# Optimization experiments

Hardware: AMD Instinct MI355X
Metric: run time of the kernel (lower is better)

Reference implementation:

```python
import jax, jax.numpy as jnp
import numpy as np

NEG_SLOPE = 0.01  # PyTorch LeakyReLU default


def leaky(x):
    return jnp.where(x >= 0, x, NEG_SLOPE * x)


def conv(x, w, b, stride, pad):
    # x: NCHW, w: OIHW
    y = jax.lax.conv_general_dilated(
        x, w, (stride, stride), [(pad, pad), (pad, pad)],
        dimension_numbers=("NCHW", "OIHW", "NCHW"))
    return y + b[None, :, None, None]


def conv_transpose(x, w, b, stride, pad):
    # w has PyTorch ConvTranspose2d layout (in, out, kh, kw)
    wf = jnp.flip(w, (2, 3)).transpose(1, 0, 2, 3)  # -> (out, in, kh, kw)
    k = w.shape[2]
    p = k - 1 - pad
    y = jax.lax.conv_general_dilated(
        x, wf, (1, 1), [(p, p), (p, p)], lhs_dilation=(stride, stride),
        dimension_numbers=("NCHW", "OIHW", "NCHW"))
    return y + b[None, :, None, None]


def setup_inputs() -> dict:
    key = jax.random.key(0)
    ks = jax.random.split(key, 16)
    D, K = 64, 512
    s = 0.05
    inp = {
        "x": jax.random.normal(ks[0], (64, 1, 128, 128), jnp.float32),
        # encoder
        "ew1": jax.random.normal(ks[1], (8, 1, 4, 4), jnp.float32) * s,
        "eb1": jnp.zeros((8,), jnp.float32),
        "ew2": jax.random.normal(ks[2], (16, 8, 4, 4), jnp.float32) * s,
        "eb2": jnp.zeros((16,), jnp.float32),
        "ew3": jax.random.normal(ks[3], (16, 16, 3, 3), jnp.float32) * s,
        "eb3": jnp.zeros((16,), jnp.float32),
        "ew4": jax.random.normal(ks[4], (D, 16, 1, 1), jnp.float32) * s,
        "eb4": jnp.zeros((D,), jnp.float32),
        # codebook, init uniform(-1/K, 1/K) as in the module
        "codebook": jax.random.uniform(ks[5], (K, D), jnp.float32, -1.0 / K, 1.0 / K),
        # decoder
        "dw1": jax.random.normal(ks[6], (16, D, 3, 3), jnp.float32) * s,
        "db1": jnp.zeros((16,), jnp.float32),
        "dw2": jax.random.normal(ks[7], (16, 8, 4, 4), jnp.float32) * s,  # ConvT (in,out,k,k)
        "db2": jnp.zeros((8,), jnp.float32),
        "dw3": jax.random.normal(ks[8], (8, 1, 4, 4), jnp.float32) * s,  # ConvT (in,out,k,k)
        "db3": jnp.zeros((1,), jnp.float32),
    }
    return inp


BETA = 0.25


def vq(latents_nchw, codebook):
    # latents -> NHWC
    lat = jnp.transpose(latents_nchw, (0, 2, 3, 1))
    shp = lat.shape
    D = shp[-1]
    flat = lat.reshape(-1, D)  # [M, D]
    # pairwise squared distances to codebook [M, K]
    dist = (jnp.sum(flat ** 2, axis=1, keepdims=True)
            + jnp.sum(codebook ** 2, axis=1)
            - 2.0 * flat @ codebook.T)
    inds = jnp.argmin(dist, axis=1)  # [M]
    quant = codebook[inds].reshape(shp)  # gather == one-hot @ codebook
    commitment_loss = jnp.mean((jax.lax.stop_gradient(quant) - lat) ** 2)
    embedding_loss = jnp.mean((quant - jax.lax.stop_gradient(lat)) ** 2)
    vq_loss = commitment_loss * BETA + embedding_loss
    # straight-through estimator
    quant = lat + jax.lax.stop_gradient(quant - lat)
    return jnp.transpose(quant, (0, 3, 1, 2)), vq_loss


def reference(x, ew1, eb1, ew2, eb2, ew3, eb3, ew4, eb4, codebook,
              dw1, db1, dw2, db2, dw3, db3):
    # encoder
    h = leaky(conv(x, ew1, eb1, 2, 1))
    h = leaky(conv(h, ew2, eb2, 2, 1))
    h = leaky(conv(h, ew3, eb3, 1, 1))
    h = leaky(conv(h, ew4, eb4, 1, 0))
    # vector quantization
    q, vq_loss = vq(h, codebook)
    # decoder
    d = leaky(conv(q, dw1, db1, 1, 1))
    d = leaky(conv_transpose(d, dw2, db2, 2, 1))
    d = jnp.tanh(conv_transpose(d, dw3, db3, 2, 1))
    return d, vq_loss
```

## Files before the change

### kernel.cpp

```cpp
#include <hip/hip_runtime.h>
#include <math.h>

#define DEV __device__ __forceinline__
DEV float leakyf(float v) { return v >= 0.f ? v : 0.01f * v; }
DEV int rfl(int v) { return __builtin_amdgcn_readfirstlane(v); }

struct F4 { float x, y, z, w; };

#define OFF_XP   0u
#define OFF_H1P  1081600u
#define OFF_H2P  3311872u
#define OFF_H3   4495616u
#define OFF_D1P  5544192u
#define OFF_D2P  6727936u
#define OFF_IDX  8958208u
#define OFF_U    9023744u
#define OFF_C2   9097472u
#define OFF_W4T  9097984u
#define OFF_DWT  9099008u
#define OFF_LOSS 9108224u

__global__ void prep_k(const float* __restrict__ ew4, const float* __restrict__ dw1,
                       const float* __restrict__ cb, float* __restrict__ ws)
{
    int b = blockIdx.x, t = threadIdx.x;
    if (b < 4) {
        int id = b * 256 + t;
        int d = id & 63, ci = id >> 6;
        ws[OFF_W4T + id] = ew4[d * 16 + ci];
    } else if (b < 6) {
        int k = (b - 4) * 256 + t;
        float s = 0.f;
        #pragma unroll
        for (int d = 0; d < 64; ++d) { float v = cb[k * 64 + d]; s = fmaf(v, v, s); }
        ws[OFF_C2 + k] = s;
    } else {
        int id = (b - 6) * 256 + t;
        if (id < 9216) {
            int co = id & 15, tap = (id >> 4) % 9, ci = id / 144;
            ws[OFF_DWT + id] = dw1[(co * 64 + ci) * 9 + tap];
        }
    }
}

__global__ void uprep_k(const float* __restrict__ dwT, const float* __restrict__ cb,
                        float* __restrict__ U)
{
    int id = blockIdx.x * 256 + threadIdx.x;
    int k = id / 144;
    int r = id - k * 144;
    float s = 0.f;
    #pragma unroll
    for (int ci = 0; ci < 64; ++ci)
        s = fmaf(cb[k * 64 + ci], dwT[ci * 144 + r], s);
    U[id] = s;
}

DEV void halo_store(float* base, int plane, int r, int W, int H, long psz)
{
    int row, col;
    if (r < W)          { row = 0;     col = r; }
    else if (r < 2 * W) { row = H - 1; col = r - W; }
    else { int r2 = r - 2 * W; row = 1 + (r2 >> 1); col = (r2 & 1) ? W - 1 : 0; }
    base[plane * psz + row * W + col] = 0.f;
}

__global__ void halo_k(float* __restrict__ ws)
{
    int id = blockIdx.x * 256 + threadIdx.x;
    if (id < 33024) {
        halo_store(ws + OFF_XP, id / 516, id % 516, 130, 130, 16900);
    } else if (id < 166144) {
        int i = id - 33024;
        halo_store(ws + OFF_H1P, i / 260, i % 260, 66, 66, 4356);
    } else if (id < 301312) {
        int i = id - 166144;
        halo_store(ws + OFF_H2P, i / 132, i % 132, 34, 34, 1156);
    } else if (id < 436480) {
        int i = id - 301312;
        halo_store(ws + OFF_D1P, i / 132, i % 132, 34, 34, 1156);
    } else if (id < 569600) {
        int i = id - 436480;
        halo_store(ws + OFF_D2P, i / 260, i % 260, 66, 66, 4356);
    }
}

__global__ void padx_k(const float* __restrict__ x, float* __restrict__ xp)
{
    int id = blockIdx.x * 256 + threadIdx.x;
    int ix = id & 127, iy = (id >> 7) & 127, n = id >> 14;
    xp[(n * 130 + iy + 1) * 130 + ix + 1] = x[id];
}

__global__ __launch_bounds__(256) void e1p_k(const float* __restrict__ xp,
                                             const float* __restrict__ ew1,
                                             const float* __restrict__ eb1,
                                             float* __restrict__ h1p)
{
    __shared__ float wl[128];
    int t = threadIdx.x;
    if (t < 128) { int co = t & 7, tap = t >> 3; wl[t] = ew1[co * 16 + tap]; }
    __syncthreads();
    int id = blockIdx.x * 256 + t;
    int x = id & 63, y = (id >> 6) & 63, n = id >> 12;
    float acc[8];
    #pragma unroll
    for (int j = 0; j < 8; ++j) acc[j] = eb1[j];
    const float* base = xp + (n * 130 + 2 * y) * 130 + 2 * x;
    #pragma unroll
    for (int ky = 0; ky < 4; ++ky) {
        F4 v = *(const F4*)(base + ky * 130);
        float vv[4] = { v.x, v.y, v.z, v.w };
        #pragma unroll
        for (int kx = 0; kx < 4; ++kx) {
            const float* wp = &wl[(ky * 4 + kx) * 8];
            #pragma unroll
            for (int j = 0; j < 8; ++j) acc[j] = fmaf(vv[kx], wp[j], acc[j]);
        }
    }
    #pragma unroll
    for (int j = 0; j < 8; ++j)
        h1p[((n * 8 + j) * 66 + y + 1) * 66 + x + 1] = leakyf(acc[j]);
}

__global__ __launch_bounds__(256) void e2p_k(const float* __restrict__ h1p,
                                             const float* __restrict__ ew2,
                                             const float* __restrict__ eb2,
                                             float* __restrict__ h2p)
{
    __shared__ float wl[512];
    int t = threadIdx.x;
    int id = blockIdx.x * 256 + t;
    int x = id & 31, y = (id >> 5) & 31;
    int cg = rfl((id >> 10) & 3), n = id >> 12;
    {
        int i = t + (t < 256 ? 0 : 0);
        for (i = t; i < 512; i += 256) {
            int co = i & 3, r = i >> 2;
            int kx = r & 3, ky = (r >> 2) & 3, ci = r >> 4;
            wl[i] = ew2[((cg * 4 + co) * 8 + ci) * 16 + ky * 4 + kx];
        }
    }
    __syncthreads();
    float acc[4];
    #pragma unroll
    for (int j = 0; j < 4; ++j) acc[j] = eb2[cg * 4 + j];
    #pragma unroll 1
    for (int ci = 0; ci < 8; ++ci) {
        const float* base = h1p + ((n * 8 + ci) * 66 + 2 * y) * 66 + 2 * x;
        #pragma unroll
        for (int ky = 0; ky < 4; ++ky) {
            F4 v = *(const F4*)(base + ky * 66);
            float vv[4] = { v.x, v.y, v.z, v.w };
            #pragma unroll
            for (int kx = 0; kx < 4; ++kx) {
                const float* wp = &wl[((ci * 4 + ky) * 4 + kx) * 4];
                acc[0] = fmaf(vv[kx], wp[0], acc[0]);
                acc[1] = fmaf(vv[kx], wp[1], acc[1]);
                acc[2] = fmaf(vv[kx], wp[2], acc[2]);
                acc[3] = fmaf(vv[kx], wp[3], acc[3]);
            }
        }
    }
    #pragma unroll
    for (int j = 0; j < 4; ++j)
        h2p[((n * 16 + cg * 4 + j) * 34 + y + 1) * 34 + x + 1] = leakyf(acc[j]);
}

__global__ __launch_bounds__(256) void e3p_k(const float* __restrict__ h2p,
                                             const float* __restrict__ ew3,
                                             const float* __restrict__ eb3,
                                             float* __restrict__ h3)
{
    __shared__ float wl[576];
    int t = threadIdx.x;
    int id = blockIdx.x * 256 + t;
    int x = id & 31, y = (id >> 5) & 31;
    int cg = rfl((id >> 10) & 3), n = id >> 12;
    for (int i = t; i < 576; i += 256) {
        int co = i & 3, r = i >> 2;
        int kx = r % 3, ky = (r / 3) % 3, ci = r / 9;
        wl[i] = ew3[((cg * 4 + co) * 16 + ci) * 9 + ky * 3 + kx];
    }
    __syncthreads();
    float acc[4];
    #pragma unroll
    for (int j = 0; j < 4; ++j) acc[j] = eb3[cg * 4 + j];
    #pragma unroll 1
    for (int ci = 0; ci < 16; ++ci) {
        const float* base = h2p + ((n * 16 + ci) * 34 + y) * 34 + x;
        #pragma unroll
        for (int ky = 0; ky < 3; ++ky) {
            F4 v = *(const F4*)(base + ky * 34);
            float vv[3] = { v.x, v.y, v.z };
            #pragma unroll
            for (int kx = 0; kx < 3; ++kx) {
                const float* wp = &wl[((ci * 3 + ky) * 3 + kx) * 4];
                acc[0] = fmaf(vv[kx], wp[0], acc[0]);
                acc[1] = fmaf(vv[kx], wp[1], acc[1]);
                acc[2] = fmaf(vv[kx], wp[2], acc[2]);
                acc[3] = fmaf(vv[kx], wp[3], acc[3]);
            }
        }
    }
    #pragma unroll
    for (int j = 0; j < 4; ++j)
        h3[((n * 16 + cg * 4 + j) << 10) + (y << 5) + x] = leakyf(acc[j]);
}

__global__ __launch_bounds__(256) void vqh_k(const float* __restrict__ h3,
                                             const float* __restrict__ w4t,
                                             const float* __restrict__ eb4,
                                             const float* __restrict__ cb,
                                             const float* __restrict__ c2,
                                             int* __restrict__ idxOut,
                                             float* __restrict__ lossAcc)
{
    __shared__ float Fs[64 * 128];
    __shared__ float Cs[64 * 128];
    int t = threadIdx.x;
    int row0 = blockIdx.x << 7;
    int n = row0 >> 10;
    int pos0 = row0 & 1023;

    {
        int row = t & 127, dh = t >> 7;
        const float* hp = h3 + (n << 14) + pos0 + row;
        float h[16];
        #pragma unroll
        for (int ci = 0; ci < 16; ++ci) h[ci] = hp[ci << 10];
        #pragma unroll
        for (int q = 0; q < 8; ++q) {
            int d0 = dh * 32 + q * 4;
            float a0 = eb4[d0 + 0], a1 = eb4[d0 + 1];
            float a2 = eb4[d0 + 2], a3 = eb4[d0 + 3];
            #pragma unroll
            for (int ci = 0; ci < 16; ++ci) {
                float v = h[ci];
                const float* wp = w4t + (ci << 6) + d0;
                a0 = fmaf(v, wp[0], a0); a1 = fmaf(v, wp[1], a1);
                a2 = fmaf(v, wp[2], a2); a3 = fmaf(v, wp[3], a3);
            }
            Fs[(d0 + 0) * 128 + row] = leakyf(a0);
            Fs[(d0 + 1) * 128 + row] = leakyf(a1);
            Fs[(d0 + 2) * 128 + row] = leakyf(a2);
            Fs[(d0 + 3) * 128 + row] = leakyf(a3);
        }
    }

    int tr = t & 15, tc = t >> 4;
    float best[8]; int bk[8];
    #pragma unroll
    for (int i = 0; i < 8; ++i) { best[i] = 3.4e38f; bk[i] = 0; }

    #pragma unroll 1
    for (int p = 0; p < 4; ++p) {
        __syncthreads();
        {
            int code = t >> 1, dh = t & 1;
            const float* src = cb + (((p << 7) + code) << 6) + dh * 32;
            #pragma unroll
            for (int q = 0; q < 8; ++q) {
                float4 v = *(const float4*)(src + q * 4);
                int d0 = dh * 32 + q * 4;
                Cs[(d0 + 0) * 128 + code] = v.x;
                Cs[(d0 + 1) * 128 + code] = v.y;
                Cs[(d0 + 2) * 128 + code] = v.z;
                Cs[(d0 + 3) * 128 + code] = v.w;
            }
        }
        __syncthreads();

        float acc[8][8];
        #pragma unroll
        for (int i = 0; i < 8; ++i)
            #pragma unroll
            for (int j = 0; j < 8; ++j) acc[i][j] = 0.f;

        const float* fp0 = &Fs[tr * 4];
        const float* fp1 = &Fs[64 + tr * 4];
        const float* cp0 = &Cs[tc * 4];
        const float* cp1 = &Cs[64 + tc * 4];
        #pragma unroll 8
        for (int d = 0; d < 64; ++d) {
            float4 f0 = *(const float4*)(fp0 + d * 128);
            float4 f1 = *(const float4*)(fp1 + d * 128);
            float4 c0 = *(const float4*)(cp0 + d * 128);
            float4 c1 = *(const float4*)(cp1 + d * 128);
            float f[8] = { f0.x, f0.y, f0.z, f0.w, f1.x, f1.y, f1.z, f1.w };
            float c[8] = { c0.x, c0.y, c0.z, c0.w, c1.x, c1.y, c1.z, c1.w };
            #pragma unroll
            for (int i = 0; i < 8; ++i)
                #pragma unroll
                for (int j = 0; j < 8; ++j)
                    acc[i][j] = fmaf(f[i], c[j], acc[i][j]);
        }
        #pragma unroll
        for (int j = 0; j < 8; ++j) {
            int kk = (p << 7) + (j < 4 ? tc * 4 + j : 64 + tc * 4 + j - 4);
            float hc2 = 0.5f * c2[kk];
            #pragma unroll
            for (int i = 0; i < 8; ++i) {
                float s = hc2 - acc[i][j];
                if (s < best[i]) { best[i] = s; bk[i] = kk; }
            }
        }
    }

    __syncthreads();
    float* redS = Cs;
    int*   redI = (int*)(Cs + 2176);
    #pragma unroll
    for (int i = 0; i < 8; ++i) {
        int row = (i < 4) ? tr * 4 + i : 64 + tr * 4 + i - 4;
        redS[row * 17 + tc] = best[i];
        redI[row * 17 + tc] = bk[i];
    }
    __syncthreads();
    if (t < 128) {
        int row = t;
        float bs = redS[row * 17]; int bi = redI[row * 17];
        #pragma unroll
        for (int c = 1; c < 16; ++c) {
            float s2 = redS[row * 17 + c];
            int   i2 = redI[row * 17 + c];
            if (s2 < bs || (s2 == bs && i2 < bi)) { bs = s2; bi = i2; }
        }
        idxOut[row0 + row] = bi;
        const float* cr = cb + (bi << 6);
        float rs = 0.f;
        #pragma unroll
        for (int d = 0; d < 64; ++d) {
            float e = cr[d] - Fs[d * 128 + row];
            rs = fmaf(e, e, rs);
        }
        #pragma unroll
        for (int off = 32; off; off >>= 1) rs += __shfl_down(rs, off, 64);
        if ((t & 63) == 0) atomicAdd(lossAcc, rs);
    }
}

__global__ __launch_bounds__(256) void d1p_k(const int* __restrict__ idx,
                                             const float* __restrict__ U,
                                             const float* __restrict__ db1,
                                             float* __restrict__ d1p)
{
    int id = blockIdx.x * 256 + threadIdx.x;
    int x = id & 31, y = (id >> 5) & 31;
    int cg = rfl((id >> 10) & 3), n = id >> 12;
    float acc[4];
    #pragma unroll
    for (int j = 0; j < 4; ++j) acc[j] = db1[cg * 4 + j];
    const float4* U4 = (const float4*)U;
    #pragma unroll
    for (int tap = 0; tap < 9; ++tap) {
        int yy = y + tap / 3 - 1, xx = x + tap % 3 - 1;
        if (yy < 0 || yy > 31 || xx < 0 || xx > 31) continue;
        int k = idx[(n << 10) + (yy << 5) + xx];
        float4 u = U4[(k * 9 + tap) * 4 + cg];
        acc[0] += u.x; acc[1] += u.y; acc[2] += u.z; acc[3] += u.w;
    }
    #pragma unroll
    for (int j = 0; j < 4; ++j)
        d1p[((n * 16 + cg * 4 + j) * 34 + y + 1) * 34 + x + 1] = leakyf(acc[j]);
}

__global__ __launch_bounds__(256) void dt2p_k(const float* __restrict__ d1p,
                                              const float* __restrict__ dw2,
                                              const float* __restrict__ db2,
                                              float* __restrict__ d2p)
{
    __shared__ float wl[512];
    int t = threadIdx.x;
    int id = blockIdx.x * 256 + t;
    int x = id & 31, y = (id >> 5) & 31;
    int cg = rfl((id >> 10) & 3), n = id >> 12;
    for (int i = t; i < 512; i += 256) {
        int co = i & 1, tap = (i >> 1) & 15, ci = i >> 5;
        wl[i] = dw2[(ci * 8 + cg * 2 + co) * 16 + tap];
    }
    __syncthreads();
    float acc[2][2][2];
    #pragma unroll
    for (int py = 0; py < 2; ++py)
        #pragma unroll
        for (int px = 0; px < 2; ++px)
            #pragma unroll
            for (int j = 0; j < 2; ++j) acc[py][px][j] = db2[cg * 2 + j];
    #pragma unroll 1
    for (int ci = 0; ci < 16; ++ci) {
        const float* base = d1p + ((n * 16 + ci) * 34 + y) * 34 + x;
        F4 r0 = *(const F4*)(base);
        F4 r1 = *(const F4*)(base + 34);
        F4 r2 = *(const F4*)(base + 68);
        float v[3][3] = { { r0.x, r0.y, r0.z },
                          { r1.x, r1.y, r1.z },
                          { r2.x, r2.y, r2.z } };
        #pragma unroll
        for (int ky = 0; ky < 4; ++ky) {
            int py = (ky + 1) & 1;
            int dy = (ky == 0) ? 1 : (ky == 3 ? -1 : 0);
            #pragma unroll
            for (int kx = 0; kx < 4; ++kx) {
                int px = (kx + 1) & 1;
                int dx = (kx == 0) ? 1 : (kx == 3 ? -1 : 0);
                float vv = v[dy + 1][dx + 1];
                const float* wp = &wl[(ci * 16 + ky * 4 + kx) * 2];
                acc[py][px][0] = fmaf(vv, wp[0], acc[py][px][0]);
                acc[py][px][1] = fmaf(vv, wp[1], acc[py][px][1]);
            }
        }
    }
    #pragma unroll
    for (int py = 0; py < 2; ++py)
        #pragma unroll
        for (int px = 0; px < 2; ++px)
            #pragma unroll
            for (int j = 0; j < 2; ++j)
                d2p[((n * 8 + cg * 2 + j) * 66 + 2 * y + py + 1) * 66 + 2 * x + px + 1] =
                    leakyf(acc[py][px][j]);
}

__global__ __launch_bounds__(256) void dt3p_k(const float* __restrict__ d2p,
                                              const float* __restrict__ dw3,
                                              const float* __restrict__ db3,
                                              float* __restrict__ out)
{
    int id = blockIdx.x * 256 + threadIdx.x;
    int x = id & 63, y = (id >> 6) & 63, n = id >> 12;
    float b = db3[0];
    float acc[2][2] = { { b, b }, { b, b } };
    #pragma unroll 1
    for (int ci = 0; ci < 8; ++ci) {
        const float* base = d2p + ((n * 8 + ci) * 66 + y) * 66 + x;
        F4 r0 = *(const F4*)(base);
        F4 r1 = *(const F4*)(base + 66);
        F4 r2 = *(const F4*)(base + 132);
        float v[3][3] = { { r0.x, r0.y, r0.z },
                          { r1.x, r1.y, r1.z },
                          { r2.x, r2.y, r2.z } };
        #pragma unroll
        for (int ky = 0; ky < 4; ++ky) {
            int py = (ky + 1) & 1;
            int dy = (ky == 0) ? 1 : (ky == 3 ? -1 : 0);
            #pragma unroll
            for (int kx = 0; kx < 4; ++kx) {
                int px = (kx + 1) & 1;
                int dx = (kx == 0) ? 1 : (kx == 3 ? -1 : 0);
                acc[py][px] = fmaf(v[dy + 1][dx + 1], dw3[ci * 16 + ky * 4 + kx],
                                   acc[py][px]);
            }
        }
    }
    #pragma unroll
    for (int py = 0; py < 2; ++py)
        #pragma unroll
        for (int px = 0; px < 2; ++px)
            out[(n << 14) + ((2 * y + py) << 7) + 2 * x + px] = tanhf(acc[py][px]);
}

__global__ void loss_k(const float* __restrict__ acc, float* __restrict__ out)
{
    out[0] = 1.25f * acc[0] / 4194304.0f;
}

extern "C" void kernel_launch(void* const* d_in, const int* in_sizes, int n_in,
                              void* d_out, int out_size, void* d_ws, size_t ws_size,
                              hipStream_t stream)
{
    const float* x        = (const float*)d_in[0];
    const float* ew1      = (const float*)d_in[1];
    const float* eb1      = (const float*)d_in[2];
    const float* ew2      = (const float*)d_in[3];
    const float* eb2      = (const float*)d_in[4];
    const float* ew3      = (const float*)d_in[5];
    const float* eb3      = (const float*)d_in[6];
    const float* ew4      = (const float*)d_in[7];
    const float* eb4      = (const float*)d_in[8];
    const float* codebook = (const float*)d_in[9];
    const float* dw1      = (const float*)d_in[10];
    const float* db1      = (const float*)d_in[11];
    const float* dw2      = (const float*)d_in[12];
    const float* db2      = (const float*)d_in[13];
    const float* dw3      = (const float*)d_in[14];
    const float* db3      = (const float*)d_in[15];

    float* out = (float*)d_out;
    float* ws  = (float*)d_ws;
    float* XP   = ws + OFF_XP;
    float* H1P  = ws + OFF_H1P;
    float* H2P  = ws + OFF_H2P;
    float* H3   = ws + OFF_H3;
    float* D1P  = ws + OFF_D1P;
    float* D2P  = ws + OFF_D2P;
    int*   IDX  = (int*)(ws + OFF_IDX);
    float* U    = ws + OFF_U;
    float* C2   = ws + OFF_C2;
    float* W4T  = ws + OFF_W4T;
    float* DWT  = ws + OFF_DWT;
    float* LOSS = ws + OFF_LOSS;

    hipMemsetAsync(LOSS, 0, sizeof(float), stream);
    prep_k<<<42, 256, 0, stream>>>(ew4, dw1, codebook, ws);
    uprep_k<<<288, 256, 0, stream>>>(DWT, codebook, U);
    halo_k<<<2225, 256, 0, stream>>>(ws);
    padx_k<<<4096, 256, 0, stream>>>(x, XP);

    e1p_k<<<1024, 256, 0, stream>>>(XP, ew1, eb1, H1P);
    e2p_k<<<1024, 256, 0, stream>>>(H1P, ew2, eb2, H2P);
    e3p_k<<<1024, 256, 0, stream>>>(H2P, ew3, eb3, H3);

    vqh_k<<<512, 256, 0, stream>>>(H3, W4T, eb4, codebook, C2, IDX, LOSS);

    d1p_k<<<1024, 256, 0, stream>>>(IDX, U, db1, D1P);
    dt2p_k<<<1024, 256, 0, stream>>>(D1P, dw2, db2, D2P);
    dt3p_k<<<1024, 256, 0, stream>>>(D2P, dw3, db3, out);

    loss_k<<<1, 1, 0, stream>>>(LOSS, out + 1048576);
}
```

Before: 148.6 us.

## Read transposed codebook from global in VQ kernel, merge setup launches

Adds a transposed codebook buffer built in the prep kernel. The VQ distance kernel now reads codebook tiles directly from global/L2 instead of staging them in shared memory, which removes the per-pass shared-memory fill and its barriers. The memset and the separate pad/halo kernels are folded into existing launches to cut launch count. The trade is that each thread now issues global loads inside the inner loop, which could add latency if L2 hits do not hide it.

```diff
diff --git a/kernel.cpp b/kernel.cpp
--- a/kernel.cpp
+++ b/kernel.cpp
@@ -19,11 +19,13 @@
 #define OFF_W4T  9097984u
 #define OFF_DWT  9099008u
 #define OFF_LOSS 9108224u
+#define OFF_CT   9108480u
 
 __global__ void prep_k(const float* __restrict__ ew4, const float* __restrict__ dw1,
                        const float* __restrict__ cb, float* __restrict__ ws)
 {
     int b = blockIdx.x, t = threadIdx.x;
+    if (b == 0 && t == 0) ws[OFF_LOSS] = 0.f;
     if (b < 4) {
         int id = b * 256 + t;
         int d = id & 63, ci = id >> 6;
@@ -34,12 +36,16 @@
         #pragma unroll
         for (int d = 0; d < 64; ++d) { float v = cb[k * 64 + d]; s = fmaf(v, v, s); }
         ws[OFF_C2 + k] = s;
-    } else {
+    } else if (b < 42) {
         int id = (b - 6) * 256 + t;
         if (id < 9216) {
             int co = id & 15, tap = (id >> 4) % 9, ci = id / 144;
             ws[OFF_DWT + id] = dw1[(co * 64 + ci) * 9 + tap];
         }
+    } else {
+        int id = (b - 42) * 256 + t;
+        int d = id >> 9, k = id & 511;
+        ws[OFF_CT + id] = cb[(k << 6) + d];
     }
 }
 
@@ -65,9 +71,13 @@
     base[plane * psz + row * W + col] = 0.f;
 }
 
-__global__ void halo_k(float* __restrict__ ws)
+__global__ void setup2_k(const float* __restrict__ x, float* __restrict__ ws)
 {
     int id = blockIdx.x * 256 + threadIdx.x;
+    {
+        int ix = id & 127, iy = (id >> 7) & 127, n = id >> 14;
+        ws[OFF_XP + (n * 130 + iy + 1) * 130 + ix + 1] = x[id];
+    }
     if (id < 33024) {
         halo_store(ws + OFF_XP, id / 516, id % 516, 130, 130, 16900);
     } else if (id < 166144) {
@@ -85,13 +95,6 @@
     }
 }
 
-__global__ void padx_k(const float* __restrict__ x, float* __restrict__ xp)
-{
-    int id = blockIdx.x * 256 + threadIdx.x;
-    int ix = id & 127, iy = (id >> 7) & 127, n = id >> 14;
-    xp[(n * 130 + iy + 1) * 130 + ix + 1] = x[id];
-}
-
 __global__ __launch_bounds__(256) void e1p_k(const float* __restrict__ xp,
                                              const float* __restrict__ ew1,
                                              const float* __restrict__ eb1,
@@ -133,13 +136,10 @@
     int id = blockIdx.x * 256 + t;
     int x = id & 31, y = (id >> 5) & 31;
     int cg = rfl((id >> 10) & 3), n = id >> 12;
-    {
-        int i = t + (t < 256 ? 0 : 0);
-        for (i = t; i < 512; i += 256) {
-            int co = i & 3, r = i >> 2;
-            int kx = r & 3, ky = (r >> 2) & 3, ci = r >> 4;
-            wl[i] = ew2[((cg * 4 + co) * 8 + ci) * 16 + ky * 4 + kx];
-        }
+    for (int i = t; i < 512; i += 256) {
+        int co = i & 3, r = i >> 2;
+        int kx = r & 3, ky = (r >> 2) & 3, ci = r >> 4;
+        wl[i] = ew2[((cg * 4 + co) * 8 + ci) * 16 + ky * 4 + kx];
     }
     __syncthreads();
     float acc[4];
@@ -208,16 +208,18 @@
         h3[((n * 16 + cg * 4 + j) << 10) + (y << 5) + x] = leakyf(acc[j]);
 }
 
-__global__ __launch_bounds__(256) void vqh_k(const float* __restrict__ h3,
+__global__ __launch_bounds__(256) void vqi_k(const float* __restrict__ h3,
                                              const float* __restrict__ w4t,
                                              const float* __restrict__ eb4,
+                                             const float* __restrict__ ct,
                                              const float* __restrict__ cb,
                                              const float* __restrict__ c2,
                                              int* __restrict__ idxOut,
                                              float* __restrict__ lossAcc)
 {
     __shared__ float Fs[64 * 128];
-    __shared__ float Cs[64 * 128];
+    __shared__ float redS[128 * 17];
+    __shared__ int   redI[128 * 17];
     int t = threadIdx.x;
     int row0 = blockIdx.x << 7;
     int n = row0 >> 10;
@@ -247,6 +249,7 @@
             Fs[(d0 + 3) * 128 + row] = leakyf(a3);
         }
     }
+    __syncthreads();
 
     int tr = t & 15, tc = t >> 4;
     float best[8]; int bk[8];
@@ -255,22 +258,6 @@
 
     #pragma unroll 1
     for (int p = 0; p < 4; ++p) {
-        __syncthreads();
-        {
-            int code = t >> 1, dh = t & 1;
-            const float* src = cb + (((p << 7) + code) << 6) + dh * 32;
-            #pragma unroll
-            for (int q = 0; q < 8; ++q) {
-                float4 v = *(const float4*)(src + q * 4);
-                int d0 = dh * 32 + q * 4;
-                Cs[(d0 + 0) * 128 + code] = v.x;
-                Cs[(d0 + 1) * 128 + code] = v.y;
-                Cs[(d0 + 2) * 128 + code] = v.z;
-                Cs[(d0 + 3) * 128 + code] = v.w;
-            }
-        }
-        __syncthreads();
-
         float acc[8][8];
         #pragma unroll
         for (int i = 0; i < 8; ++i)
@@ -279,14 +266,14 @@
 
         const float* fp0 = &Fs[tr * 4];
         const float* fp1 = &Fs[64 + tr * 4];
-        const float* cp0 = &Cs[tc * 4];
-        const float* cp1 = &Cs[64 + tc * 4];
+        const float* cp0 = ct + (p << 7) + tc * 4;
+        const float* cp1 = cp0 + 64;
         #pragma unroll 8
         for (int d = 0; d < 64; ++d) {
+            float4 c0 = *(const float4*)(cp0 + d * 512);
+            float4 c1 = *(const float4*)(cp1 + d * 512);
             float4 f0 = *(const float4*)(fp0 + d * 128);
             float4 f1 = *(const float4*)(fp1 + d * 128);
-            float4 c0 = *(const float4*)(cp0 + d * 128);
-            float4 c1 = *(const float4*)(cp1 + d * 128);
             float f[8] = { f0.x, f0.y, f0.z, f0.w, f1.x, f1.y, f1.z, f1.w };
             float c[8] = { c0.x, c0.y, c0.z, c0.w, c1.x, c1.y, c1.z, c1.w };
             #pragma unroll
@@ -307,9 +294,6 @@
         }
     }
 
-    __syncthreads();
-    float* redS = Cs;
-    int*   redI = (int*)(Cs + 2176);
     #pragma unroll
     for (int i = 0; i < 8; ++i) {
         int row = (i < 4) ? tr * 4 + i : 64 + tr * 4 + i - 4;
@@ -499,18 +483,17 @@
     float* W4T  = ws + OFF_W4T;
     float* DWT  = ws + OFF_DWT;
     float* LOSS = ws + OFF_LOSS;
-
-    hipMemsetAsync(LOSS, 0, sizeof(float), stream);
-    prep_k<<<42, 256, 0, stream>>>(ew4, dw1, codebook, ws);
+    float* CT   = ws + OFF_CT;
+
+    prep_k<<<170, 256, 0, stream>>>(ew4, dw1, codebook, ws);
     uprep_k<<<288, 256, 0, stream>>>(DWT, codebook, U);
-    halo_k<<<2225, 256, 0, stream>>>(ws);
-    padx_k<<<4096, 256, 0, stream>>>(x, XP);
+    setup2_k<<<4096, 256, 0, stream>>>(x, ws);
 
     e1p_k<<<1024, 256, 0, stream>>>(XP, ew1, eb1, H1P);
     e2p_k<<<1024, 256, 0, stream>>>(H1P, ew2, eb2, H2P);
     e3p_k<<<1024, 256, 0, stream>>>(H2P, ew3, eb3, H3);
 
-    vqh_k<<<512, 256, 0, stream>>>(H3, W4T, eb4, codebook, C2, IDX, LOSS);
+    vqi_k<<<512, 256, 0, stream>>>(H3, W4T, eb4, CT, codebook, C2, IDX, LOSS);
 
     d1p_k<<<1024, 256, 0, stream>>>(IDX, U, db1, D1P);
     dt2p_k<<<1024, 256, 0, stream>>>(D1P, dw2, db2, D2P);
```

New measurement: 174.3 us. +17.3%, slower.
